# Optimization experiments

Hardware: AMD Instinct MI355X
Metric: run time of the kernel (lower is better)

## Reference

```python
import math
import jax, jax.numpy as jnp
import numpy as np

K_TOP = 8
D_HEAD = 32


def causal_topk_adjacency(x, K):
    # Binary adjacency: for each position t, top-K strictly-causal (j < t)
    # neighbours by dot-product similarity. Rows with < K valid positions
    # (e.g. t=0 has none) get only their valid entries (possibly zero rows).
    B, T, D = x.shape
    sim = jnp.einsum('btd,bsd->bts', x, x) / math.sqrt(D)  # (B,T,T)
    causal = jnp.tril(jnp.ones((T, T), dtype=bool), k=-1)   # j < t
    neg = jnp.finfo(sim.dtype).min
    sim_m = jnp.where(causal[None], sim, neg)
    vals, idx = jax.lax.top_k(sim_m, K)                      # (B,T,K)
    valid = (vals > neg).astype(x.dtype)
    b = jnp.arange(B)[:, None, None]
    t = jnp.arange(T)[None, :, None]
    A = jnp.zeros((B, T, T), x.dtype).at[b, t, idx].max(valid)
    return A


def setup_inputs() -> dict:
    key = jax.random.key(0)
    ks = jax.random.split(key, 3)
    B, T, D = 2, 4096, 1024
    x = jax.random.normal(ks[0], (B, T, D), dtype=jnp.float32)
    W_q = jax.random.normal(ks[1], (D_HEAD, D), dtype=jnp.float32) * (1.0 / math.sqrt(D))
    W_k = jax.random.normal(ks[2], (D_HEAD, D), dtype=jnp.float32) * (1.0 / math.sqrt(D))
    gain = jnp.ones((D,), dtype=jnp.float32)
    bias = jnp.zeros((D,), dtype=jnp.float32)
    log_mix = jnp.zeros((), dtype=jnp.float32)
    log_scale = jnp.zeros((), dtype=jnp.float32)
    return {"x": x, "W_q": W_q, "W_k": W_k, "gain": gain, "bias": bias,
            "log_mix": log_mix, "log_scale": log_scale}


def reference(x, W_q, W_k, gain, bias, log_mix, log_scale):
    B, T, D = x.shape
    mix = jax.nn.sigmoid(log_mix)
    scale = jax.nn.softplus(log_scale) + 0.01

    A = causal_topk_adjacency(x, K_TOP)                      # (B,T,T) binary

    q = jnp.einsum('btd,hd->bth', x, W_q)                    # (B,T,Dh)
    k = jnp.einsum('bsd,hd->bsh', x, W_k)
    score = jnp.einsum('bth,bsh->bts', q, k) / math.sqrt(D_HEAD)
    score = jnp.where(A < 0.5, -1e9, score)

    row_max = jax.lax.stop_gradient(jnp.max(score, axis=-1, keepdims=True))
    score = score - row_max
    attn = jax.nn.softmax(score, axis=-1)
    attn = jnp.nan_to_num(attn, nan=0.0)

    msg = jnp.einsum('bts,bsd->btd', attn, x)
    blended = mix * x + (1.0 - mix) * msg
    delta = jax.nn.gelu(blended * gain + bias, approximate=False) * scale
    return delta
```

## Files before the change

### kernel.cpp

```cpp
#include <hip/hip_runtime.h>
#include <math.h>

#define B 2
#define T 4096
#define D 1024
#define DH 32
#define TNB 32
#define NBLK 528
#define NK 12
#define CPR (32*NK)

typedef __bf16 bf16x8 __attribute__((ext_vector_type(8)));
typedef float f32x4 __attribute__((ext_vector_type(4)));

#define AS1 __attribute__((address_space(1)))
#define AS3 __attribute__((address_space(3)))

__device__ __forceinline__ unsigned mono32(float v) {
    unsigned u = __float_as_uint(v);
    u ^= ((unsigned)((int)u >> 31)) | 0x80000000u;
    return u;
}

__device__ __forceinline__ unsigned dpp_umax_bcast(unsigned v) {
    #define DPPMAX(CTRL) { unsigned t_ = (unsigned)__builtin_amdgcn_update_dpp(0, (int)v, CTRL, 0xF, 0xF, true); v = v > t_ ? v : t_; }
    DPPMAX(0x111) DPPMAX(0x112) DPPMAX(0x114) DPPMAX(0x118)
    DPPMAX(0x142) DPPMAX(0x143)
    #undef DPPMAX
    return (unsigned)__builtin_amdgcn_readlane((int)v, 63);
}
__device__ __forceinline__ float dpp_fsum_bcast(float v) {
    #define DPPADD(CTRL) { int t_ = __builtin_amdgcn_update_dpp(0, __float_as_int(v), CTRL, 0xF, 0xF, true); v += __int_as_float(t_); }
    DPPADD(0x111) DPPADD(0x112) DPPADD(0x114) DPPADD(0x118)
    DPPADD(0x142) DPPADD(0x143)
    #undef DPPADD
    return __int_as_float(__builtin_amdgcn_readlane(__float_as_int(v), 63));
}
__device__ __forceinline__ float dpp_gsum8(float p) {
    { int t_ = __builtin_amdgcn_update_dpp(0, __float_as_int(p), 0x0B1, 0xF, 0xF, true); p += __int_as_float(t_); }
    { int t_ = __builtin_amdgcn_update_dpp(0, __float_as_int(p), 0x04E, 0xF, 0xF, true); p += __int_as_float(t_); }
    { int t_ = __builtin_amdgcn_update_dpp(0, __float_as_int(p), 0x141, 0xF, 0xF, true); p += __int_as_float(t_); }
    return p;
}

__device__ __forceinline__ void merge12(const unsigned* a12, const unsigned* b12,
                                        unsigned* o12) {
    unsigned m16[16];
    #pragma unroll
    for (int i = 0; i < 16; ++i) {
        unsigned aa = (i < NK) ? a12[i] : 0u;
        unsigned bb = (15 - i < NK) ? b12[15 - i] : 0u;
        m16[i] = aa > bb ? aa : bb;
    }
    #pragma unroll
    for (int g = 8; g >= 1; g >>= 1) {
        #pragma unroll
        for (int i = 0; i < 16; ++i) {
            if (!(i & g)) {
                unsigned x0 = m16[i], x1 = m16[i + g];
                m16[i]     = x0 > x1 ? x0 : x1;
                m16[i + g] = x0 > x1 ? x1 : x0;
            }
        }
    }
    #pragma unroll
    for (int i = 0; i < NK; ++i) o12[i] = m16[i];
}

__global__ __launch_bounds__(256) void conv_kernel(const float* __restrict__ x,
        __bf16* __restrict__ xhi, __bf16* __restrict__ xlo)
{
    int i = (blockIdx.x * 256 + threadIdx.x) << 3;
    float4 a = *(const float4*)(x + i);
    float4 c = *(const float4*)(x + i + 4);
    float av[8] = {a.x, a.y, a.z, a.w, c.x, c.y, c.z, c.w};
    __bf16 h[8], l[8];
    #pragma unroll
    for (int j = 0; j < 8; ++j) {
        h[j] = (__bf16)av[j];
        l[j] = (__bf16)(av[j] - (float)h[j]);
    }
    *(float4*)(xhi + i) = *(float4*)h;
    *(float4*)(xlo + i) = *(float4*)l;
}

__global__ void mean_kernel(const float* __restrict__ x, float* __restrict__ meansum)
{
    int gid  = blockIdx.x;
    int b    = gid >> 6;
    int rem  = gid & 63;
    int dblk = rem >> 4;
    int tch  = rem & 15;
    int d = dblk * 256 + threadIdx.x;
    const float* xp = x + (b * T + tch * 256) * D + d;
    float s = 0.f;
    #pragma unroll 8
    for (int it = 0; it < 256; ++it) s += xp[it * D];
    atomicAdd(&meansum[(b << 10) + d], s);
}

__global__ __launch_bounds__(256) void qk_mfma_kernel(
        const __bf16* __restrict__ xhi, const __bf16* __restrict__ xlo,
        const __bf16* __restrict__ Whi, const __bf16* __restrict__ Wlo,
        float* __restrict__ qo, float* __restrict__ ko)
{
    __shared__ __align__(16) __bf16 stg[10240];
    __bf16* sAhi = stg;
    __bf16* sAlo = stg + 2560;
    __bf16* sBhi = stg + 5120;
    __bf16* sBlo = stg + 7680;

    int tid = threadIdx.x;
    int m0 = blockIdx.x << 6;
    int w = tid >> 6, lane = tid & 63;
    int fr = lane & 15, fq = lane >> 4;

    int arow = tid >> 2, aq = tid & 3;
    const __bf16* gAh = xhi + (size_t)(m0 + arow) * D + aq * 8;
    const __bf16* gAl = xlo + (size_t)(m0 + arow) * D + aq * 8;
    const __bf16* gBh = Whi + arow * D + aq * 8;
    const __bf16* gBl = Wlo + arow * D + aq * 8;

    f32x4 acc[4];
    #pragma unroll
    for (int j = 0; j < 4; ++j) acc[j] = (f32x4){0.f, 0.f, 0.f, 0.f};

    float4 a0 = *(const float4*)(gAh);
    float4 a1 = *(const float4*)(gAl);
    float4 b0 = *(const float4*)(gBh);
    float4 b1 = *(const float4*)(gBl);

    int sa = arow * 40 + aq * 8;

    for (int kc = 0; kc < 32; ++kc) {
        __syncthreads();
        *(float4*)(sAhi + sa) = a0;
        *(float4*)(sAlo + sa) = a1;
        *(float4*)(sBhi + sa) = b0;
        *(float4*)(sBlo + sa) = b1;
        __syncthreads();
        if (kc + 1 < 32) {
            int k0 = (kc + 1) << 5;
            a0 = *(const float4*)(gAh + k0);
            a1 = *(const float4*)(gAl + k0);
            b0 = *(const float4*)(gBh + k0);
            b1 = *(const float4*)(gBl + k0);
        }
        int r = (w << 4) + fr;
        bf16x8 fah = *(const bf16x8*)(sAhi + r * 40 + fq * 8);
        bf16x8 fal = *(const bf16x8*)(sAlo + r * 40 + fq * 8);
        bf16x8 fbh[4], fbl[4];
        #pragma unroll
        for (int j = 0; j < 4; ++j) {
            int rb = j * 16 + fr;
            fbh[j] = *(const bf16x8*)(sBhi + rb * 40 + fq * 8);
            fbl[j] = *(const bf16x8*)(sBlo + rb * 40 + fq * 8);
        }
        #pragma unroll
        for (int j = 0; j < 4; ++j) {
            acc[j] = __builtin_amdgcn_mfma_f32_16x16x32_bf16(fah, fbh[j], acc[j], 0, 0, 0);
            acc[j] = __builtin_amdgcn_mfma_f32_16x16x32_bf16(fah, fbl[j], acc[j], 0, 0, 0);
            acc[j] = __builtin_amdgcn_mfma_f32_16x16x32_bf16(fal, fbh[j], acc[j], 0, 0, 0);
        }
    }
    int grow0 = m0 + (w << 4) + (fq << 2);
    #pragma unroll
    for (int j = 0; j < 4; ++j) {
        int gn = j * 16 + fr;
        float* dst = (gn < 32) ? (qo + grow0 * DH + gn)
                               : (ko + grow0 * DH + gn - 32);
        dst[0]      = acc[j][0];
        dst[DH]     = acc[j][1];
        dst[2 * DH] = acc[j][2];
        dst[3 * DH] = acc[j][3];
    }
}

__global__ __launch_bounds__(256, 4) void topk_mfma_kernel(
        const __bf16* __restrict__ xhi, unsigned* __restrict__ pkey)
{
    __shared__ __align__(16) char smem[49152];
    __bf16* stg = (__bf16*)smem;
    float* Sbuf = (float*)smem;
    unsigned* kbuf = (unsigned*)(smem + 33024);

    int tid = threadIdx.x;
    int b = blockIdx.x / NBLK;
    int l = blockIdx.x - b * NBLK;
    int rt = (int)((sqrtf(8.f * l + 1.f) - 1.f) * 0.5f);
    while ((rt + 1) * (rt + 2) / 2 <= l) ++rt;
    while (rt * (rt + 1) / 2 > l) --rt;
    int ct = l - rt * (rt + 1) / 2;
    int r0 = rt << 7, c0 = ct << 7;
    int base = b * T;

    int w = tid >> 6, lane = tid & 63;
    int wr = (w >> 1) << 6, wc = (w & 1) << 6;
    bool active = !(rt == ct && w == 1);
    int fr = lane & 15, fq = lane >> 4;
    int fqs = (fq ^ ((fr >> 1) & 3)) << 3;

    int lrow = lane >> 2;
    int lcq = (((lane & 3) ^ ((lane >> 3) & 3)) << 3);
    const __bf16* gA = xhi + (size_t)(base + r0) * D;
    const __bf16* gB = xhi + (size_t)(base + c0) * D;
    const __bf16* gA0 = gA + (size_t)((w << 4) + lrow) * D + lcq;
    const __bf16* gA1 = gA0 + (size_t)64 * D;
    const __bf16* gB0 = gB + (size_t)((w << 4) + lrow) * D + lcq;
    const __bf16* gB1 = gB0 + (size_t)64 * D;

    f32x4 acc[4][4];
    #pragma unroll
    for (int i = 0; i < 4; ++i)
        #pragma unroll
        for (int j = 0; j < 4; ++j) acc[i][j] = (f32x4){0.f, 0.f, 0.f, 0.f};

#define ISSUE_TILE(BUFBASE, KO) do { \
    __bf16* bA_ = (BUFBASE); \
    __bf16* bB_ = bA_ + 4096; \
    __builtin_amdgcn_global_load_lds((const AS1 unsigned int*)(gA0 + (KO)), \
        (AS3 unsigned int*)(bA_ + (w << 9)), 16, 0, 0); \
    __builtin_amdgcn_global_load_lds((const AS1 unsigned int*)(gA1 + (KO)), \
        (AS3 unsigned int*)(bA_ + 2048 + (w << 9)), 16, 0, 0); \
    __builtin_amdgcn_global_load_lds((const AS1 unsigned int*)(gB0 + (KO)), \
        (AS3 unsigned int*)(bB_ + (w << 9)), 16, 0, 0); \
    __builtin_amdgcn_global_load_lds((const AS1 unsigned int*)(gB1 + (KO)), \
        (AS3 unsigned int*)(bB_ + 2048 + (w << 9)), 16, 0, 0); \
} while (0)

    ISSUE_TILE(stg, 0);
    ISSUE_TILE(stg + 8192, 32);

    int bsel = 0, isel = 2;
    for (int kc = 0; kc < 32; ++kc) {
        if (kc < 31) { asm volatile("s_waitcnt vmcnt(4)" ::: "memory"); }
        else         { asm volatile("s_waitcnt vmcnt(0)" ::: "memory"); }
        __builtin_amdgcn_s_barrier();
        asm volatile("" ::: "memory");
        if (kc + 2 < 32) {
            ISSUE_TILE(stg + isel * 8192, (kc + 2) << 5);
            isel = (isel == 2) ? 0 : isel + 1;
        }
        if (active) {
            const __bf16* cA = stg + bsel * 8192;
            const __bf16* cB = cA + 4096;
            bf16x8 ah[4], bh[4];
            #pragma unroll
            for (int i = 0; i < 4; ++i) {
                int ar = wr + i * 16 + fr;
                ah[i] = *(const bf16x8*)(cA + ar * 32 + fqs);
                int bc = wc + i * 16 + fr;
                bh[i] = *(const bf16x8*)(cB + bc * 32 + fqs);
            }
            #pragma unroll
            for (int i = 0; i < 4; ++i)
                #pragma unroll
                for (int j = 0; j < 4; ++j)
                    acc[i][j] = __builtin_amdgcn_mfma_f32_16x16x32_bf16(ah[i], bh[j], acc[i][j], 0, 0, 0);
        }
        bsel = (bsel == 2) ? 0 : bsel + 1;
    }
#undef ISSUE_TILE

    int cr = fq << 2, cc = fr;
    #pragma unroll
    for (int phase = 0; phase < 2; ++phase) {
        __syncthreads();
        if ((w >> 1) == phase) {
            #pragma unroll
            for (int i = 0; i < 4; ++i)
                #pragma unroll
                for (int j = 0; j < 4; ++j) {
                    float* sp = Sbuf + (i * 16 + cr) * 129 + wc + j * 16 + cc;
                    sp[0]       = acc[i][j][0];
                    sp[129]     = acc[i][j][1];
                    sp[2 * 129] = acc[i][j][2];
                    sp[3 * 129] = acc[i][j][3];
                }
        }
        __syncthreads();
        {
            int row = tid & 63, qtr = tid >> 6;
            int gt = r0 + (phase << 6) + row;
            int cmax = gt - c0;
            if (cmax > 128) cmax = 128;
            if (cmax < 0) cmax = 0;
            int h0 = qtr << 5;
            int hmax = cmax < (h0 + 32) ? cmax : (h0 + 32);
            unsigned key[NK];
            #pragma unroll
            for (int i = 0; i < NK; ++i) key[i] = 0u;
            const float* Srow = Sbuf + row * 129;
            for (int cb = h0; cb < hmax; cb += 8) {
                float v[8];
                #pragma unroll
                for (int j = 0; j < 8; ++j) v[j] = Srow[cb + j];
                #pragma unroll
                for (int j = 0; j < 8; ++j) {
                    int c = cb + j;
                    unsigned u = mono32(v[j]);
                    unsigned tk = (c < hmax) ? ((u & 0xFFFFFF80u) | (unsigned)(127 - c)) : 0u;
                    #pragma unroll
                    for (int i = 0; i < NK; ++i) {
                        unsigned hi = key[i] > tk ? key[i] : tk;
                        unsigned lo = key[i] > tk ? tk : key[i];
                        key[i] = hi; tk = lo;
                    }
                }
            }
            #pragma unroll
            for (int i = 0; i < NK; ++i) kbuf[tid * 13 + i] = key[i];
        }
        __syncthreads();
        if (tid < 128) {
            int r = tid & 63, hf = tid >> 6;
            int ia = r + (hf << 7);
            unsigned a12[NK], b12[NK], o12[NK];
            #pragma unroll
            for (int i = 0; i < NK; ++i) {
                a12[i] = kbuf[ia * 13 + i];
                b12[i] = kbuf[(ia + 64) * 13 + i];
            }
            merge12(a12, b12, o12);
            #pragma unroll
            for (int i = 0; i < NK; ++i) kbuf[ia * 13 + i] = o12[i];
        }
        __syncthreads();
        if (tid < 64) {
            unsigned a12[NK], b12[NK], o12[NK];
            #pragma unroll
            for (int i = 0; i < NK; ++i) {
                a12[i] = kbuf[tid * 13 + i];
                b12[i] = kbuf[(tid + 128) * 13 + i];
            }
            merge12(a12, b12, o12);
            int gt = r0 + (phase << 6) + tid;
            int ob = (base + gt) * CPR + ct * NK;
            #pragma unroll
            for (int i = 0; i < NK; ++i) {
                unsigned kk = o12[i];
                int gcol = c0 + 127 - (int)(kk & 127u);
                pkey[ob + i] = kk ? ((kk & 0xFFFFF000u) | (unsigned)(4095 - gcol)) : 0u;
            }
        }
    }
}

__global__ __launch_bounds__(256) void select_msg_kernel(const float* __restrict__ x,
        const float* __restrict__ q, const float* __restrict__ k,
        const float* __restrict__ meansum,
        const unsigned* __restrict__ pkey,
        const float* __restrict__ gain, const float* __restrict__ bias,
        const float* __restrict__ plm, const float* __restrict__ pls,
        float* __restrict__ out)
{
    int tid = threadIdx.x;
    int w = tid >> 6, lane = tid & 63;
    int rid = (blockIdx.x << 2) + w;
    int b = rid >> 12, t = rid & (T - 1);
    int ncand = NK * ((t + 127) >> 7);

    unsigned cv[6];
    #pragma unroll
    for (int u = 0; u < 6; ++u) {
        int cid = lane + (u << 6);
        cv[u] = (cid < ncand) ? pkey[(size_t)rid * CPR + cid] : 0u;
    }
    const float* xt = x + (size_t)rid * D;
    float4 xt4[4];
    #pragma unroll
    for (int c = 0; c < 4; ++c)
        xt4[c] = *(const float4*)(xt + (c << 8) + (lane << 2));

    unsigned skey[NK]; int sgid[NK];
    #pragma unroll
    for (int i = 0; i < NK; ++i) {
        unsigned m = cv[0];
        #pragma unroll
        for (int u = 1; u < 6; ++u) m = m > cv[u] ? m : cv[u];
        m = dpp_umax_bcast(m);
        skey[i] = m;
        sgid[i] = 4095 - (int)(m & 4095u);
        #pragma unroll
        for (int u = 0; u < 6; ++u) cv[u] = (cv[u] == m) ? 0u : cv[u];
    }

    float ex[NK];
    #pragma unroll
    for (int batch = 0; batch < 3; ++batch) {
        float4 rv[4][4];
        #pragma unroll
        for (int s = 0; s < 4; ++s) {
            int i = batch * 4 + s;
            int row = (skey[i] != 0u) ? sgid[i] : 0;
            const float* xj = x + (size_t)((b << 12) + row) * D;
            #pragma unroll
            for (int c = 0; c < 4; ++c)
                rv[s][c] = *(const float4*)(xj + (c << 8) + (lane << 2));
        }
        #pragma unroll
        for (int s = 0; s < 4; ++s) {
            float ss = 0.f;
            #pragma unroll
            for (int c = 0; c < 4; ++c)
                ss += xt4[c].x * rv[s][c].x + xt4[c].y * rv[s][c].y
                    + xt4[c].z * rv[s][c].z + xt4[c].w * rv[s][c].w;
            ex[batch * 4 + s] = dpp_fsum_bcast(ss);
        }
    }

    unsigned long long top8[8];
    #pragma unroll
    for (int r = 0; r < 8; ++r) top8[r] = 0ull;
    #pragma unroll
    for (int i = 0; i < NK; ++i) {
        unsigned u = mono32(ex[i]);
        unsigned long long t64 = (skey[i] != 0u)
            ? ((((unsigned long long)u) << 12) | (unsigned long long)(4095 - sgid[i]))
            : 0ull;
        #pragma unroll
        for (int r = 0; r < 8; ++r) {
            unsigned long long hi = (t64 > top8[r]) ? t64 : top8[r];
            unsigned long long lo = (t64 > top8[r]) ? top8[r] : t64;
            top8[r] = hi; t64 = lo;
        }
    }
    bool vld[8]; int bidx[8];
    #pragma unroll
    for (int i = 0; i < 8; ++i) {
        vld[i]  = top8[i] != 0ull;
        bidx[i] = 4095 - (int)(top8[i] & 4095ull);
    }

    int i8 = lane >> 3, e = lane & 7;
    unsigned long long kk = (i8 & 4)
        ? ((i8 & 2) ? ((i8 & 1) ? top8[7] : top8[6]) : ((i8 & 1) ? top8[5] : top8[4]))
        : ((i8 & 2) ? ((i8 & 1) ? top8[3] : top8[2]) : ((i8 & 1) ? top8[1] : top8[0]));
    bool v8 = kk != 0ull;
    int g8 = v8 ? (4095 - (int)(kk & 4095ull)) : 0;
    float4 qv = *(const float4*)(q + (size_t)rid * DH + (e << 2));
    float4 kv = *(const float4*)(k + (size_t)((b << 12) + g8) * DH + (e << 2));
    float p = qv.x * kv.x + qv.y * kv.y + qv.z * kv.z + qv.w * kv.w;
    p = dpp_gsum8(p);
    p *= 0.17677669529663687f;

    float sc[8];
    #pragma unroll
    for (int i = 0; i < 8; ++i)
        sc[i] = __int_as_float(__builtin_amdgcn_readlane(__float_as_int(p), i << 3));

    float m = -INFINITY; int cnt = 0;
    #pragma unroll
    for (int i = 0; i < 8; ++i)
        if (vld[i]) { ++cnt; if (sc[i] > m) m = sc[i]; }

    float wgt[8]; float Z = 0.f; int gsel[8];
    #pragma unroll
    for (int i = 0; i < 8; ++i) {
        wgt[i] = vld[i] ? expf(sc[i] - m) : 0.f;
        Z += wgt[i];
        gsel[i] = vld[i] ? ((b << 12) + bidx[i]) : (b << 12);
    }
    float invZ = (cnt > 0) ? 1.f / Z : 0.f;
    #pragma unroll
    for (int i = 0; i < 8; ++i) wgt[i] *= invZ;

    float mix   = 1.f / (1.f + expf(-plm[0]));
    float scale = log1pf(expf(pls[0])) + 0.01f;
    const float onemix = 1.f - mix;

    float4 msg4[4];
    if (cnt == 0) {
        #pragma unroll
        for (int c = 0; c < 4; ++c) {
            float4 ms = *(const float4*)(meansum + (b << 10) + (c << 8) + (lane << 2));
            msg4[c].x = ms.x * (1.f / (float)T); msg4[c].y = ms.y * (1.f / (float)T);
            msg4[c].z = ms.z * (1.f / (float)T); msg4[c].w = ms.w * (1.f / (float)T);
        }
    } else {
        #pragma unroll
        for (int c = 0; c < 4; ++c) msg4[c] = (float4){0.f, 0.f, 0.f, 0.f};
        #pragma unroll
        for (int g = 0; g < 2; ++g) {
            float4 rv[4][4];
            #pragma unroll
            for (int s = 0; s < 4; ++s) {
                const float* xj = x + (size_t)gsel[g * 4 + s] * D;
                #pragma unroll
                for (int c = 0; c < 4; ++c)
                    rv[s][c] = *(const float4*)(xj + (c << 8) + (lane << 2));
            }
            #pragma unroll
            for (int s = 0; s < 4; ++s) {
                float wi = wgt[g * 4 + s];
                #pragma unroll
                for (int c = 0; c < 4; ++c) {
                    msg4[c].x += wi * rv[s][c].x; msg4[c].y += wi * rv[s][c].y;
                    msg4[c].z += wi * rv[s][c].z; msg4[c].w += wi * rv[s][c].w;
                }
            }
        }
    }
    #pragma unroll
    for (int c = 0; c < 4; ++c) {
        int d0 = (c << 8) + (lane << 2);
        float4 g4 = *(const float4*)(gain + d0);
        float4 b4 = *(const float4*)(bias + d0);
        float4 xv = xt4[c];
        float zi[4] = {
            (mix * xv.x + onemix * msg4[c].x) * g4.x + b4.x,
            (mix * xv.y + onemix * msg4[c].y) * g4.y + b4.y,
            (mix * xv.z + onemix * msg4[c].z) * g4.z + b4.z,
            (mix * xv.w + onemix * msg4[c].w) * g4.w + b4.w };
        float4 o4;
        o4.x = 0.5f * zi[0] * (1.f + erff(zi[0] * 0.70710678118654752f)) * scale;
        o4.y = 0.5f * zi[1] * (1.f + erff(zi[1] * 0.70710678118654752f)) * scale;
        o4.z = 0.5f * zi[2] * (1.f + erff(zi[2] * 0.70710678118654752f)) * scale;
        o4.w = 0.5f * zi[3] * (1.f + erff(zi[3] * 0.70710678118654752f)) * scale;
        *(float4*)(out + (size_t)rid * D + d0) = o4;
    }
}

extern "C" void kernel_launch(void* const* d_in, const int* in_sizes, int n_in,
                              void* d_out, int out_size, void* d_ws, size_t ws_size,
                              hipStream_t stream)
{
    const float* x    = (const float*)d_in[0];
    const float* Wq   = (const float*)d_in[1];
    const float* Wk   = (const float*)d_in[2];
    const float* gain = (const float*)d_in[3];
    const float* bias = (const float*)d_in[4];
    const float* plm  = (const float*)d_in[5];
    const float* pls  = (const float*)d_in[6];
    float* out = (float*)d_out;

    float* ws      = (float*)d_ws;
    float* q       = ws;
    float* k       = ws + 262144;
    float* meansum = ws + 524288;
    unsigned* pkey = (unsigned*)(ws + 526336);
    __bf16* xhi    = (__bf16*)(ws + 3672064);
    __bf16* xlo    = xhi + (size_t)B * T * D;
    __bf16* Whi    = xlo + (size_t)B * T * D;
    __bf16* Wlo    = Whi + 64 * D;

    hipMemsetAsync(meansum, 0, 2048 * sizeof(float), stream);
    conv_kernel<<<B * T * D / 2048, 256, 0, stream>>>(x, xhi, xlo);
    conv_kernel<<<16, 256, 0, stream>>>(Wq, Whi, Wlo);
    conv_kernel<<<16, 256, 0, stream>>>(Wk, Whi + 32 * D, Wlo + 32 * D);
    mean_kernel<<<128, 256, 0, stream>>>(x, meansum);
    qk_mfma_kernel<<<B * T / 64, 256, 0, stream>>>(xhi, xlo, Whi, Wlo, q, k);
    topk_mfma_kernel<<<B * NBLK, 256, 0, stream>>>(xhi, pkey);
    select_msg_kernel<<<B * T / 4, 256, 0, stream>>>(x, q, k, meansum, pkey,
                                                     gain, bias, plm, pls, out);
}
```

Measured before the change: 267.5 us.

## Shrink topk kernel LDS with double buffering and two-way row split

Staging in the top-k MFMA kernel drops from a triple buffer to a double buffer. A second barrier is added after the MFMAs so the next tile can be issued into the buffer just consumed. The per-row top-k scan now uses 128 threads covering 64 columns each instead of 256 threads covering 32, which removes one merge round and its sync. Shared memory falls to about 39 KB, which should let more blocks sit on each CU. The cost is an extra barrier per k-step, less load/compute overlap, and half the threads idle during the insertion sort.

```diff
diff --git a/kernel.cpp b/kernel.cpp
--- a/kernel.cpp
+++ b/kernel.cpp
@@ -179,7 +179,7 @@
 __global__ __launch_bounds__(256, 4) void topk_mfma_kernel(
         const __bf16* __restrict__ xhi, unsigned* __restrict__ pkey)
 {
-    __shared__ __align__(16) char smem[49152];
+    __shared__ __align__(16) char smem[39680];
     __bf16* stg = (__bf16*)smem;
     float* Sbuf = (float*)smem;
     unsigned* kbuf = (unsigned*)(smem + 33024);
@@ -231,18 +231,13 @@
     ISSUE_TILE(stg, 0);
     ISSUE_TILE(stg + 8192, 32);
 
-    int bsel = 0, isel = 2;
     for (int kc = 0; kc < 32; ++kc) {
         if (kc < 31) { asm volatile("s_waitcnt vmcnt(4)" ::: "memory"); }
         else         { asm volatile("s_waitcnt vmcnt(0)" ::: "memory"); }
         __builtin_amdgcn_s_barrier();
         asm volatile("" ::: "memory");
-        if (kc + 2 < 32) {
-            ISSUE_TILE(stg + isel * 8192, (kc + 2) << 5);
-            isel = (isel == 2) ? 0 : isel + 1;
-        }
         if (active) {
-            const __bf16* cA = stg + bsel * 8192;
+            const __bf16* cA = stg + ((kc & 1) << 13);
             const __bf16* cB = cA + 4096;
             bf16x8 ah[4], bh[4];
             #pragma unroll
@@ -258,7 +253,11 @@
                 for (int j = 0; j < 4; ++j)
                     acc[i][j] = __builtin_amdgcn_mfma_f32_16x16x32_bf16(ah[i], bh[j], acc[i][j], 0, 0, 0);
         }
-        bsel = (bsel == 2) ? 0 : bsel + 1;
+        asm volatile("" ::: "memory");
+        __builtin_amdgcn_s_barrier();
+        asm volatile("" ::: "memory");
+        if (kc + 2 < 32)
+            ISSUE_TILE(stg + ((kc & 1) << 13), (kc + 2) << 5);
     }
 #undef ISSUE_TILE
 
@@ -279,14 +278,14 @@
                 }
         }
         __syncthreads();
-        {
-            int row = tid & 63, qtr = tid >> 6;
+        if (tid < 128) {
+            int row = tid & 63, half = tid >> 6;
             int gt = r0 + (phase << 6) + row;
             int cmax = gt - c0;
             if (cmax > 128) cmax = 128;
             if (cmax < 0) cmax = 0;
-            int h0 = qtr << 5;
-            int hmax = cmax < (h0 + 32) ? cmax : (h0 + 32);
+            int h0 = half << 6;
+            int hmax = cmax < (h0 + 64) ? cmax : (h0 + 64);
             unsigned key[NK];
             #pragma unroll
             for (int i = 0; i < NK; ++i) key[i] = 0u;
@@ -312,26 +311,12 @@
             for (int i = 0; i < NK; ++i) kbuf[tid * 13 + i] = key[i];
         }
         __syncthreads();
-        if (tid < 128) {
-            int r = tid & 63, hf = tid >> 6;
-            int ia = r + (hf << 7);
-            unsigned a12[NK], b12[NK], o12[NK];
-            #pragma unroll
-            for (int i = 0; i < NK; ++i) {
-                a12[i] = kbuf[ia * 13 + i];
-                b12[i] = kbuf[(ia + 64) * 13 + i];
-            }
-            merge12(a12, b12, o12);
-            #pragma unroll
-            for (int i = 0; i < NK; ++i) kbuf[ia * 13 + i] = o12[i];
-        }
-        __syncthreads();
         if (tid < 64) {
             unsigned a12[NK], b12[NK], o12[NK];
             #pragma unroll
             for (int i = 0; i < NK; ++i) {
                 a12[i] = kbuf[tid * 13 + i];
-                b12[i] = kbuf[(tid + 128) * 13 + i];
+                b12[i] = kbuf[(tid + 64) * 13 + i];
             }
             merge12(a12, b12, o12);
             int gt = r0 + (phase << 6) + tid;
```

New measurement: 274.1 us. +2.5%, slower.
